# Optimization experiments

Hardware: AMD Instinct MI355X
Metric: run time of the kernel (lower is better)

## Reference

```python
import jax, jax.numpy as jnp
import numpy as np

WS = 7       # window size
SHIFT = 3    # shift size (ws//2)
NH = 16      # num heads
DIM = 512    # channels
HH = 112
WW = 112
HIDDEN = int(DIM * 4.0)
EPS = 1e-5


def _rel_index():
    # Swin relative position index, [N, N] ints into the bias table
    coords = np.stack(np.meshgrid(np.arange(WS), np.arange(WS), indexing='ij')).reshape(2, -1)
    rel = coords[:, :, None] - coords[:, None, :]
    rel = rel.transpose(1, 2, 0) + (WS - 1)
    rel[:, :, 0] *= 2 * WS - 1
    return rel.sum(-1)


def _attn_mask():
    # shifted-window mask on HH x WW (already multiples of WS) -> [nW, N, N] with 0 / -1e9
    img = np.zeros((HH, WW), np.int32)
    cnt = 0
    sl = (slice(0, -WS), slice(-WS, -SHIFT), slice(-SHIFT, None))
    for h in sl:
        for w in sl:
            img[h, w] = cnt
            cnt += 1
    win = img.reshape(HH // WS, WS, WW // WS, WS).transpose(0, 2, 1, 3).reshape(-1, WS * WS)
    diff = win[:, None, :] - win[:, :, None]
    return np.where(diff == 0, 0.0, -1e9).astype(np.float32)


def setup_inputs() -> dict:
    key = jax.random.key(0)
    ks = jax.random.split(key, 8)
    s = 0.02
    return {
        'x': jax.random.normal(ks[0], (DIM, HH, WW), jnp.float32),
        'norm1_w': jnp.ones((DIM,), jnp.float32),
        'norm1_b': jnp.zeros((DIM,), jnp.float32),
        'qkv_w': jax.random.normal(ks[1], (3 * DIM, DIM), jnp.float32) * s,
        'qkv_b': jnp.zeros((3 * DIM,), jnp.float32),
        'proj_w': jax.random.normal(ks[2], (DIM, DIM), jnp.float32) * s,
        'proj_b': jnp.zeros((DIM,), jnp.float32),
        'rpb_table': jax.random.normal(ks[3], ((2 * WS - 1) ** 2, NH), jnp.float32) * s,
        'norm2_w': jnp.ones((DIM,), jnp.float32),
        'norm2_b': jnp.zeros((DIM,), jnp.float32),
        'fc1_w': jax.random.normal(ks[4], (HIDDEN, DIM), jnp.float32) * s,
        'fc1_b': jnp.zeros((HIDDEN,), jnp.float32),
        'fc2_w': jax.random.normal(ks[5], (DIM, HIDDEN), jnp.float32) * s,
        'fc2_b': jnp.zeros((DIM,), jnp.float32),
    }


def _ln(x_hwc, w, b):
    m = x_hwc.mean(-1, keepdims=True)
    v = x_hwc.var(-1, keepdims=True)
    return (x_hwc - m) / jnp.sqrt(v + EPS) * w + b


def reference(x, norm1_w, norm1_b, qkv_w, qkv_b, proj_w, proj_b, rpb_table,
              norm2_w, norm2_b, fc1_w, fc1_b, fc2_w, fc2_b):
    C, H, W = x.shape
    ws = WS
    N = ws * ws
    hd = C // NH
    scale = 1.0 / np.sqrt(hd).astype(np.float32)

    x_hwc = jnp.moveaxis(x, 0, -1)                       # [H,W,C]
    xn = _ln(x_hwc, norm1_w, norm1_b)
    xs = jnp.roll(xn, (-SHIFT, -SHIFT), (0, 1))          # cyclic shift
    # window partition -> [nW, N, C]
    xw = xs.reshape(H // ws, ws, W // ws, ws, C).transpose(0, 2, 1, 3, 4).reshape(-1, N, C)

    qkv = xw @ qkv_w.T + qkv_b                            # [nW,N,3C]
    q, k, v = jnp.split(qkv, 3, -1)
    heads = lambda t: t.reshape(-1, N, NH, hd).transpose(0, 2, 1, 3)  # [nW,H,N,hd]
    q, k, v = heads(q), heads(k), heads(v)

    attn = jnp.einsum('whnd,whmd->whnm', q * scale, k)    # [nW,H,N,N]
    idx = jnp.asarray(_rel_index().reshape(-1))
    bias = rpb_table[idx].reshape(N, N, NH).transpose(2, 0, 1)  # [H,N,N]
    mask = jnp.asarray(_attn_mask())                       # [nW,N,N]
    attn = attn + bias[None] + mask[:, None]
    attn = jax.nn.softmax(attn, -1)

    out = jnp.einsum('whnm,whmd->whnd', attn, v).transpose(0, 2, 1, 3).reshape(-1, N, C)
    out = out @ proj_w.T + proj_b
    # window unpartition + reverse shift
    out = out.reshape(H // ws, W // ws, ws, ws, C).transpose(0, 2, 1, 3, 4).reshape(H, W, C)
    out = jnp.roll(out, (SHIFT, SHIFT), (0, 1))

    x1 = x_hwc + out                                       # residual (DropPath rate 0)
    x2 = _ln(x1, norm2_w, norm2_b)
    h = jax.nn.gelu(x2.reshape(-1, C) @ fc1_w.T + fc1_b)
    m = (h @ fc2_w.T + fc2_b).reshape(H, W, C)
    y = x1 + m
    return jnp.moveaxis(y, -1, 0)                          # back to [C,H,W]
```

## Files before the change

kernel.cpp:

```cpp
#include <hip/hip_runtime.h>

#define NPIX 12544
#define CDIM 512
#define QKVN 1536
#define HIDDEN 2048

typedef unsigned short u16;
typedef unsigned int u32;

typedef short bf16x8 __attribute__((ext_vector_type(8)));
typedef float f32x4 __attribute__((ext_vector_type(4)));

static __device__ __forceinline__ u16 f2bf(float f) {
  u32 u = __float_as_uint(f);
  return (u16)((u + 0x7fffu + ((u >> 16) & 1u)) >> 16);
}
static __device__ __forceinline__ u32 pack2(float a, float b) {
  return (u32)f2bf(a) | ((u32)f2bf(b) << 16);
}
static __device__ __forceinline__ u32 packtrunc2(float lo, float hi) {
  return __builtin_amdgcn_perm(__float_as_uint(hi), __float_as_uint(lo), 0x07060302u);
}
static __device__ __forceinline__ void async_ld16(const void* g, void* l) {
  __builtin_amdgcn_global_load_lds((__attribute__((address_space(1))) void*)g,
                                   (__attribute__((address_space(3))) void*)l, 16, 0, 0);
}

__global__ __launch_bounds__(256) void convert_weights(
    const float* __restrict__ qw, const float* __restrict__ pw,
    const float* __restrict__ w1, const float* __restrict__ w2,
    u16* __restrict__ Wq, u16* __restrict__ Wp, u16* __restrict__ W1o, u16* __restrict__ W2o) {
  const int b = blockIdx.x;
  const float* src; u16* dst; long off;
  if (b < 768)       { src = qw; dst = Wq;  off = (long)b * 1024; }
  else if (b < 1024) { src = pw; dst = Wp;  off = (long)(b - 768) * 1024; }
  else if (b < 2048) { src = w1; dst = W1o; off = (long)(b - 1024) * 1024; }
  else               { src = w2; dst = W2o; off = (long)(b - 2048) * 1024; }
  const long i = off / 4 + threadIdx.x;
  const float4 v = ((const float4*)src)[i];
  ushort4 u;
  u.x = f2bf(v.x); u.y = f2bf(v.y); u.z = f2bf(v.z); u.w = f2bf(v.w);
  ((ushort4*)dst)[i] = u;
}

__global__ __launch_bounds__(256) void ln1_partial(const float* __restrict__ x,
                                                   float* __restrict__ psum, float* __restrict__ pssq) {
  const int p = blockIdx.x * 256 + threadIdx.x;
  const int c0 = blockIdx.y * 32;
  float s = 0.f, ss = 0.f;
#pragma unroll
  for (int c = 0; c < 32; c++) {
    const float v = x[(long)(c0 + c) * NPIX + p];
    s += v; ss += v * v;
  }
  psum[blockIdx.y * NPIX + p] = s;
  pssq[blockIdx.y * NPIX + p] = ss;
}

__global__ __launch_bounds__(256) void ln1_stats(const float* __restrict__ psum, const float* __restrict__ pssq,
                                                 float* __restrict__ mean, float* __restrict__ rstd) {
  const int p = blockIdx.x * 256 + threadIdx.x;
  float s = 0.f, ss = 0.f;
#pragma unroll
  for (int ch = 0; ch < 16; ch++) { s += psum[ch * NPIX + p]; ss += pssq[ch * NPIX + p]; }
  const float m = s * (1.f / 512.f);
  const float v = ss * (1.f / 512.f) - m * m;
  mean[p] = m;
  rstd[p] = rsqrtf(v + 1e-5f);
}

__global__ __launch_bounds__(256) void ln1_shift_part(const float* __restrict__ x,
    const float* __restrict__ mean, const float* __restrict__ rstd,
    const float* __restrict__ gw, const float* __restrict__ gb, u16* __restrict__ xw) {
  __shared__ float tile[32][65];
  const int p0 = blockIdx.x * 64;
  const int c0 = blockIdx.y * 32;
  const int t = threadIdx.x;
  {
    const int pl = t & 63;
    const int cl0 = t >> 6;
#pragma unroll
    for (int r = 0; r < 8; r++) {
      const int cl = r * 4 + cl0;
      tile[cl][pl] = x[(long)(c0 + cl) * NPIX + p0 + pl];
    }
  }
  __syncthreads();
  const int cl = t & 31;
  const int g = t >> 5;
  const float wc = gw[c0 + cl];
  const float bc = gb[c0 + cl];
#pragma unroll
  for (int pass = 0; pass < 8; pass++) {
    const int pl = pass * 8 + g;
    const int p = p0 + pl;
    const int h = p / 112;
    const int w = p - h * 112;
    int hs = h + 109; if (hs >= 112) hs -= 112;
    int ws2 = w + 109; if (ws2 >= 112) ws2 -= 112;
    const int hq = hs / 7, wq = ws2 / 7;
    const int tok = (hq * 16 + wq) * 49 + (hs - hq * 7) * 7 + (ws2 - wq * 7);
    const float val = (tile[cl][pl] - mean[p]) * rstd[p] * wc + bc;
    xw[(long)tok * 512 + c0 + cl] = f2bf(val);
  }
}

template<bool OUT_BF16, bool DO_GELU, bool REMAP, bool FUSE_Y, bool FUSE_X>
__global__ __launch_bounds__(256, 3) void gemm_bt(
    const u16* __restrict__ A, const u16* __restrict__ B,
    const float* __restrict__ bias, void* __restrict__ out,
    const float* __restrict__ xtra, const int N, const int K) {
  __shared__ __align__(16) u16 Asm[128 * 32];
  __shared__ __align__(16) u16 Bsm[128 * 32];
  const int M0 = blockIdx.y << 7;
  const int N0 = blockIdx.x << 7;
  const int t = threadIdx.x;
  const int wave = t >> 6;
  const int lane = t & 63;
  const int l15 = lane & 15;
  const int quad = lane >> 4;
  const int wm = wave & 1;
  const int wn = wave >> 1;
  const int swz = (l15 >> 1) & 3;

  f32x4 acc[4][4] = {};

  for (int k0 = 0; k0 < K; k0 += 32) {
#pragma unroll
    for (int i = 0; i < 2; i++) {
      const int flatbase = i * 256 + wave * 64;
      const int FL = flatbase + lane;
      const int row = FL >> 2;
      const int chunk = (FL & 3) ^ ((row >> 1) & 3);
      async_ld16(A + (long)(M0 + row) * K + k0 + chunk * 8, &Asm[flatbase * 8]);
      async_ld16(B + (long)(N0 + row) * K + k0 + chunk * 8, &Bsm[flatbase * 8]);
    }
    __syncthreads();
    bf16x8 af[4], bfr[4];
#pragma unroll
    for (int im = 0; im < 4; im++)
      af[im] = *(const bf16x8*)&Asm[(wm * 64 + im * 16 + l15) * 32 + (quad ^ swz) * 8];
#pragma unroll
    for (int in = 0; in < 4; in++)
      bfr[in] = *(const bf16x8*)&Bsm[(wn * 64 + in * 16 + l15) * 32 + (quad ^ swz) * 8];
#pragma unroll
    for (int im = 0; im < 4; im++)
#pragma unroll
      for (int in = 0; in < 4; in++)
        acc[im][in] = __builtin_amdgcn_mfma_f32_16x16x32_bf16(bfr[in], af[im], acc[im][in], 0, 0, 0);
    __syncthreads();
  }

#pragma unroll
  for (int im = 0; im < 4; im++) {
    const int row = M0 + wm * 64 + im * 16 + l15;
    long orow = row;
    if (REMAP) {
      const int win = row / 49;
      const int nn = row - win * 49;
      const int nq = nn / 7;
      const int hs = (win >> 4) * 7 + nq;
      const int wsx = (win & 15) * 7 + (nn - nq * 7);
      int h = hs + 3; if (h >= 112) h -= 112;
      int w = wsx + 3; if (w >= 112) w -= 112;
      orow = h * 112 + w;
    }
#pragma unroll
    for (int in = 0; in < 4; in++) {
      const int col0 = N0 + wn * 64 + in * 16 + quad * 4;
      const float4 bv = *(const float4*)(bias + col0);
      float v[4];
      if (FUSE_Y) {
        const float4 xv = *(const float4*)(xtra + (long)row * CDIM + col0);
#pragma unroll
        for (int r = 0; r < 4; r++)
          v[r] = acc[im][in][r] + ((const float*)&bv)[r] + ((const float*)&xv)[r];
#pragma unroll
        for (int r = 0; r < 4; r++)
          ((float*)out)[(long)(col0 + r) * NPIX + row] = v[r];
      } else if (FUSE_X) {
        float v0 = acc[im][in][0] + bv.x + xtra[(long)(col0 + 0) * NPIX + orow];
        float v1 = acc[im][in][1] + bv.y + xtra[(long)(col0 + 1) * NPIX + orow];
        float v2 = acc[im][in][2] + bv.z + xtra[(long)(col0 + 2) * NPIX + orow];
        float v3 = acc[im][in][3] + bv.w + xtra[(long)(col0 + 3) * NPIX + orow];
        float4 f; f.x = v0; f.y = v1; f.z = v2; f.w = v3;
        *(float4*)((float*)out + orow * (long)N + col0) = f;
      } else {
#pragma unroll
        for (int r = 0; r < 4; r++) {
          float vv = acc[im][in][r] + ((const float*)&bv)[r];
          if (DO_GELU) {
            const float z2 = 1.5957691216f * (vv + 0.044715f * vv * vv * vv);
            vv = vv / (1.0f + __expf(-z2));
          }
          v[r] = vv;
        }
        if (OUT_BF16) {
          uint2 u;
          u.x = pack2(v[0], v[1]);
          u.y = pack2(v[2], v[3]);
          *(uint2*)((u16*)out + orow * (long)N + col0) = u;
        } else {
          float4 f; f.x = v[0]; f.y = v[1]; f.z = v[2]; f.w = v[3];
          *(float4*)((float*)out + orow * (long)N + col0) = f;
        }
      }
    }
  }
}

__global__ __launch_bounds__(256) void build_biasT(const float* __restrict__ rpb, float* __restrict__ biasT) {
  const int cls = blockIdx.x >> 4;
  const int head = blockIdx.x & 15;
  for (int e = threadIdx.x; e < 4096; e += 256) {
    const int j = e >> 6;
    const int i = e & 63;
    float v;
    if (j >= 49) v = -1e9f;
    else if (i >= 49) v = 0.f;
    else {
      const int ri = i / 7, ci = i - (i / 7) * 7;
      const int rj = j / 7, cj = j - (j / 7) * 7;
      v = rpb[((ri - rj + 6) * 13 + (ci - cj + 6)) * 16 + head];
      const int lhi = (cls & 2) ? (ri < 4 ? 1 : 2) : 0;
      const int lwi = (cls & 1) ? (ci < 4 ? 1 : 2) : 0;
      const int lhj = (cls & 2) ? (rj < 4 ? 1 : 2) : 0;
      const int lwj = (cls & 1) ? (cj < 4 ? 1 : 2) : 0;
      if (lhi * 3 + lwi != lhj * 3 + lwj) v = -1e9f;
    }
    biasT[(long)blockIdx.x * 4096 + e] = v;
  }
}

__global__ __launch_bounds__(256, 3) void attn_mfma(
    const u16* __restrict__ qkv, const float* __restrict__ biasT, u16* __restrict__ out) {
  __shared__ __align__(16) u16 slds[24576];
  const int t = threadIdx.x;
  const int wave = t >> 6;
  const int lane = t & 63;
  const int l15 = lane & 15;
  const int quad = lane >> 4;
  const int win = blockIdx.x >> 2;
  const int head = (blockIdx.x & 3) * 4 + wave;
  const int cls = (((win >> 4) == 15) ? 2 : 0) | (((win & 15) == 15) ? 1 : 0);

  u16* Qb  = slds + wave * 6144;
  u16* Kb  = Qb + 2048;
  u16* Vtb = Qb + 4096;
  u16* Pb  = Qb;

  const int rrow = lane >> 2;
  const int chunk = (lane & 3) ^ ((lane >> 3) & 3);
  uint4 vv[4];
#pragma unroll
  for (int it = 0; it < 4; it++) {
    const int row = it * 16 + rrow;
    const int jc = row < 49 ? row : 48;
    const long gbase = (long)(win * 49 + jc) * 1536 + head * 32 + chunk * 8;
    async_ld16(qkv + gbase,       Qb + it * 512 + lane * 8);
    async_ld16(qkv + gbase + 512, Kb + it * 512 + lane * 8);
    vv[it] = *(const uint4*)(qkv + gbase + 1024);
  }
  __syncthreads();

#pragma unroll
  for (int it = 0; it < 4; it++) {
    const int row = it * 16 + rrow;
    const u32* w = (const u32*)&vv[it];
#pragma unroll
    for (int tt = 0; tt < 8; tt++) {
      const int d = chunk * 8 + tt;
      const u16 val = (tt & 1) ? (u16)(w[tt >> 1] >> 16) : (u16)(w[tt >> 1] & 0xffffu);
      Vtb[d * 64 + (row ^ (((d >> 2) & 3) << 4))] = val;
    }
  }

  const int fswz = (l15 >> 1) & 3;
  bf16x8 kfrag[4], qfrag[4];
#pragma unroll
  for (int jm = 0; jm < 4; jm++)
    kfrag[jm] = *(const bf16x8*)(Kb + (jm * 16 + l15) * 32 + (quad ^ fswz) * 8);
#pragma unroll
  for (int in = 0; in < 4; in++)
    qfrag[in] = *(const bf16x8*)(Qb + (in * 16 + l15) * 32 + (quad ^ fswz) * 8);
  f32x4 sacc[4][4] = {};
#pragma unroll
  for (int jm = 0; jm < 4; jm++)
#pragma unroll
    for (int in = 0; in < 4; in++)
      sacc[jm][in] = __builtin_amdgcn_mfma_f32_16x16x32_bf16(kfrag[jm], qfrag[in], sacc[jm][in], 0, 0, 0);

  const float* bT = biasT + (long)(cls * 16 + head) * 4096;
  const float sc = 0.17677669529663687f;
#pragma unroll
  for (int jm = 0; jm < 4; jm++) {
    const float* bp = bT + (jm * 16 + quad * 4) * 64 + l15;
#pragma unroll
    for (int in = 0; in < 4; in++)
#pragma unroll
      for (int r = 0; r < 4; r++)
        sacc[jm][in][r] = sacc[jm][in][r] * sc + bp[r * 64 + in * 16];
  }
  float linv[4];
#pragma unroll
  for (int in = 0; in < 4; in++) {
    float m = -1e30f;
#pragma unroll
    for (int jm = 0; jm < 4; jm++)
#pragma unroll
      for (int r = 0; r < 4; r++) m = fmaxf(m, sacc[jm][in][r]);
    m = fmaxf(m, __shfl_xor(m, 16));
    m = fmaxf(m, __shfl_xor(m, 32));
    float s = 0.f;
#pragma unroll
    for (int jm = 0; jm < 4; jm++)
#pragma unroll
      for (int r = 0; r < 4; r++) {
        const float e = __expf(sacc[jm][in][r] - m);
        sacc[jm][in][r] = e; s += e;
      }
    s += __shfl_xor(s, 16);
    s += __shfl_xor(s, 32);
    linv[in] = __builtin_amdgcn_rcpf(s);
  }

#pragma unroll
  for (int in = 0; in < 4; in++) {
    const int i = in * 16 + l15;
    const int rot = (l15 & 3) << 4;
#pragma unroll
    for (int jm = 0; jm < 4; jm++) {
      const u32 lo = packtrunc2(sacc[jm][in][0], sacc[jm][in][1]);
      const u32 hi = packtrunc2(sacc[jm][in][2], sacc[jm][in][3]);
      uint2 u; u.x = lo; u.y = hi;
      *(uint2*)(Pb + i * 64 + ((jm * 16 + quad * 4) ^ rot)) = u;
    }
  }

  f32x4 oacc[2][4] = {};
#pragma unroll
  for (int ks = 0; ks < 2; ks++) {
    bf16x8 vtf[2], pf[4];
#pragma unroll
    for (int dm = 0; dm < 2; dm++)
      vtf[dm] = *(const bf16x8*)(Vtb + (dm * 16 + l15) * 64 + ((ks * 32 + quad * 8) ^ ((l15 >> 2) << 4)));
#pragma unroll
    for (int in = 0; in < 4; in++)
      pf[in] = *(const bf16x8*)(Pb + (in * 16 + l15) * 64 + ((ks * 32 + quad * 8) ^ ((l15 & 3) << 4)));
#pragma unroll
    for (int dm = 0; dm < 2; dm++)
#pragma unroll
      for (int in = 0; in < 4; in++)
        oacc[dm][in] = __builtin_amdgcn_mfma_f32_16x16x32_bf16(vtf[dm], pf[in], oacc[dm][in], 0, 0, 0);
  }

#pragma unroll
  for (int in = 0; in < 4; in++) {
    const int i = in * 16 + l15;
    if (i < 49) {
      const float inv = linv[in];
      const long base = (long)(win * 49 + i) * 512 + head * 32 + quad * 4;
#pragma unroll
      for (int dm = 0; dm < 2; dm++) {
        const float v0 = oacc[dm][in][0] * inv, v1 = oacc[dm][in][1] * inv;
        const float v2 = oacc[dm][in][2] * inv, v3 = oacc[dm][in][3] * inv;
        uint2 u; u.x = packtrunc2(v0, v1); u.y = packtrunc2(v2, v3);
        *(uint2*)(out + base + dm * 16) = u;
      }
    }
  }
}

__global__ __launch_bounds__(256) void ln2_apply(const float* __restrict__ x1,
    const float* __restrict__ gw, const float* __restrict__ gb, u16* __restrict__ x2) {
  const int wave = threadIdx.x >> 6;
  const int lane = threadIdx.x & 63;
  const int p = blockIdx.x * 4 + wave;
  const float4* row = (const float4*)(x1 + (long)p * 512);
  const float4 a = row[lane * 2];
  const float4 b = row[lane * 2 + 1];
  float s = a.x + a.y + a.z + a.w + b.x + b.y + b.z + b.w;
  float ss = a.x * a.x + a.y * a.y + a.z * a.z + a.w * a.w
           + b.x * b.x + b.y * b.y + b.z * b.z + b.w * b.w;
#pragma unroll
  for (int o = 32; o > 0; o >>= 1) { s += __shfl_xor(s, o); ss += __shfl_xor(ss, o); }
  const float m = s * (1.f / 512.f);
  const float var = ss * (1.f / 512.f) - m * m;
  const float rs = rsqrtf(var + 1e-5f);
  const float4 w0 = ((const float4*)gw)[lane * 2];
  const float4 w1 = ((const float4*)gw)[lane * 2 + 1];
  const float4 b0 = ((const float4*)gb)[lane * 2];
  const float4 b1 = ((const float4*)gb)[lane * 2 + 1];
  uint4 u;
  u.x = pack2((a.x - m) * rs * w0.x + b0.x, (a.y - m) * rs * w0.y + b0.y);
  u.y = pack2((a.z - m) * rs * w0.z + b0.z, (a.w - m) * rs * w0.w + b0.w);
  u.z = pack2((b.x - m) * rs * w1.x + b1.x, (b.y - m) * rs * w1.y + b1.y);
  u.w = pack2((b.z - m) * rs * w1.z + b1.z, (b.w - m) * rs * w1.w + b1.w);
  ((uint4*)(x2 + (long)p * 512))[lane] = u;
}

extern "C" void kernel_launch(void* const* d_in, const int* in_sizes, int n_in,
                              void* d_out, int out_size, void* d_ws, size_t ws_size,
                              hipStream_t stream) {
  (void)in_sizes; (void)n_in; (void)out_size; (void)ws_size;
  const float* x      = (const float*)d_in[0];
  const float* n1w    = (const float*)d_in[1];
  const float* n1b    = (const float*)d_in[2];
  const float* qkv_w  = (const float*)d_in[3];
  const float* qkv_b  = (const float*)d_in[4];
  const float* proj_w = (const float*)d_in[5];
  const float* proj_b = (const float*)d_in[6];
  const float* rpb    = (const float*)d_in[7];
  const float* n2w    = (const float*)d_in[8];
  const float* n2b    = (const float*)d_in[9];
  const float* fc1_w  = (const float*)d_in[10];
  const float* fc1_b  = (const float*)d_in[11];
  const float* fc2_w  = (const float*)d_in[12];
  const float* fc2_b  = (const float*)d_in[13];
  float* y = (float*)d_out;

  char* base = (char*)d_ws;
  size_t off = 0;
  auto alloc = [&](size_t b) { char* p = base + off; off += (b + 255) & ~(size_t)255; return p; };
  float* mean1 = (float*)alloc((size_t)NPIX * 4);
  float* rstd1 = (float*)alloc((size_t)NPIX * 4);
  float* psum  = (float*)alloc((size_t)16 * NPIX * 4);
  float* pssq  = (float*)alloc((size_t)16 * NPIX * 4);
  u16* Wq = (u16*)alloc((size_t)QKVN * CDIM * 2);
  u16* Wp = (u16*)alloc((size_t)CDIM * CDIM * 2);
  u16* W1 = (u16*)alloc((size_t)HIDDEN * CDIM * 2);
  u16* W2 = (u16*)alloc((size_t)CDIM * HIDDEN * 2);
  float* biasT = (float*)alloc((size_t)4 * 16 * 4096 * 4);
  u16* bufA = (u16*)alloc((size_t)NPIX * CDIM * 2);
  char* bufB = alloc((size_t)NPIX * QKVN * 2);
  float* x1 = (float*)alloc((size_t)NPIX * CDIM * 4);
  u16* hbuf = (u16*)alloc((size_t)NPIX * HIDDEN * 2);

  u16* xw      = bufA;
  u16* qkvbuf  = (u16*)bufB;
  u16* attnout = bufA;
  u16* x2 = bufA;

  convert_weights<<<3072, 256, 0, stream>>>(qkv_w, proj_w, fc1_w, fc2_w, Wq, Wp, W1, W2);
  build_biasT<<<64, 256, 0, stream>>>(rpb, biasT);

  ln1_partial<<<dim3(49, 16), 256, 0, stream>>>(x, psum, pssq);
  ln1_stats<<<49, 256, 0, stream>>>(psum, pssq, mean1, rstd1);
  ln1_shift_part<<<dim3(196, 16), 256, 0, stream>>>(x, mean1, rstd1, n1w, n1b, xw);

  gemm_bt<true, false, false, false, false><<<dim3(QKVN / 128, 98), 256, 0, stream>>>(xw, Wq, qkv_b, qkvbuf, nullptr, QKVN, CDIM);
  attn_mfma<<<1024, 256, 0, stream>>>(qkvbuf, biasT, attnout);
  gemm_bt<false, false, true, false, true><<<dim3(CDIM / 128, 98), 256, 0, stream>>>(attnout, Wp, proj_b, x1, x, CDIM, CDIM);

  ln2_apply<<<NPIX / 4, 256, 0, stream>>>(x1, n2w, n2b, x2);

  gemm_bt<true, true, false, false, false><<<dim3(HIDDEN / 128, 98), 256, 0, stream>>>(x2, W1, fc1_b, hbuf, nullptr, HIDDEN, CDIM);
  gemm_bt<false, false, false, true, false><<<dim3(CDIM / 128, 98), 256, 0, stream>>>(hbuf, W2, fc2_b, y, x1, CDIM, HIDDEN);
}
```

Measured before the change: 317.2 us.

## Fuse setup and LN1 kernels, remap GEMM tiles for XCD locality

```diff
diff --git a/kernel.cpp b/kernel.cpp
--- a/kernel.cpp
+++ b/kernel.cpp
@@ -4,6 +4,7 @@
 #define CDIM 512
 #define QKVN 1536
 #define HIDDEN 2048
+#define MT 98
 
 typedef unsigned short u16;
 typedef unsigned int u32;
@@ -26,82 +27,116 @@
                                    (__attribute__((address_space(3))) void*)l, 16, 0, 0);
 }
 
-__global__ __launch_bounds__(256) void convert_weights(
+__global__ __launch_bounds__(256) void setup_kernel(
     const float* __restrict__ qw, const float* __restrict__ pw,
     const float* __restrict__ w1, const float* __restrict__ w2,
-    u16* __restrict__ Wq, u16* __restrict__ Wp, u16* __restrict__ W1o, u16* __restrict__ W2o) {
+    const float* __restrict__ rpb,
+    u16* __restrict__ Wq, u16* __restrict__ Wp, u16* __restrict__ W1o, u16* __restrict__ W2o,
+    float* __restrict__ biasT) {
   const int b = blockIdx.x;
-  const float* src; u16* dst; long off;
-  if (b < 768)       { src = qw; dst = Wq;  off = (long)b * 1024; }
-  else if (b < 1024) { src = pw; dst = Wp;  off = (long)(b - 768) * 1024; }
-  else if (b < 2048) { src = w1; dst = W1o; off = (long)(b - 1024) * 1024; }
-  else               { src = w2; dst = W2o; off = (long)(b - 2048) * 1024; }
-  const long i = off / 4 + threadIdx.x;
-  const float4 v = ((const float4*)src)[i];
-  ushort4 u;
-  u.x = f2bf(v.x); u.y = f2bf(v.y); u.z = f2bf(v.z); u.w = f2bf(v.w);
-  ((ushort4*)dst)[i] = u;
-}
-
-__global__ __launch_bounds__(256) void ln1_partial(const float* __restrict__ x,
-                                                   float* __restrict__ psum, float* __restrict__ pssq) {
-  const int p = blockIdx.x * 256 + threadIdx.x;
-  const int c0 = blockIdx.y * 32;
-  float s = 0.f, ss = 0.f;
-#pragma unroll
-  for (int c = 0; c < 32; c++) {
-    const float v = x[(long)(c0 + c) * NPIX + p];
-    s += v; ss += v * v;
-  }
-  psum[blockIdx.y * NPIX + p] = s;
-  pssq[blockIdx.y * NPIX + p] = ss;
-}
-
-__global__ __launch_bounds__(256) void ln1_stats(const float* __restrict__ psum, const float* __restrict__ pssq,
-                                                 float* __restrict__ mean, float* __restrict__ rstd) {
-  const int p = blockIdx.x * 256 + threadIdx.x;
-  float s = 0.f, ss = 0.f;
-#pragma unroll
-  for (int ch = 0; ch < 16; ch++) { s += psum[ch * NPIX + p]; ss += pssq[ch * NPIX + p]; }
-  const float m = s * (1.f / 512.f);
-  const float v = ss * (1.f / 512.f) - m * m;
-  mean[p] = m;
-  rstd[p] = rsqrtf(v + 1e-5f);
-}
-
-__global__ __launch_bounds__(256) void ln1_shift_part(const float* __restrict__ x,
-    const float* __restrict__ mean, const float* __restrict__ rstd,
+  if (b < 3072) {
+    const float* src; u16* dst; long off;
+    if (b < 768)       { src = qw; dst = Wq;  off = (long)b * 1024; }
+    else if (b < 1024) { src = pw; dst = Wp;  off = (long)(b - 768) * 1024; }
+    else if (b < 2048) { src = w1; dst = W1o; off = (long)(b - 1024) * 1024; }
+    else               { src = w2; dst = W2o; off = (long)(b - 2048) * 1024; }
+    const long i = off / 4 + threadIdx.x;
+    const float4 v = ((const float4*)src)[i];
+    ushort4 u;
+    u.x = f2bf(v.x); u.y = f2bf(v.y); u.z = f2bf(v.z); u.w = f2bf(v.w);
+    ((ushort4*)dst)[i] = u;
+  } else {
+    const int bb = b - 3072;
+    const int cls = bb >> 4;
+    const int head = bb & 15;
+    for (int e = threadIdx.x; e < 4096; e += 256) {
+      const int j = e >> 6;
+      const int i = e & 63;
+      float v;
+      if (j >= 49) v = -1e9f;
+      else if (i >= 49) v = 0.f;
+      else {
+        const int ri = i / 7, ci = i - (i / 7) * 7;
+        const int rj = j / 7, cj = j - (j / 7) * 7;
+        v = rpb[((ri - rj + 6) * 13 + (ci - cj + 6)) * 16 + head];
+        const int lhi = (cls & 2) ? (ri < 4 ? 1 : 2) : 0;
+        const int lwi = (cls & 1) ? (ci < 4 ? 1 : 2) : 0;
+        const int lhj = (cls & 2) ? (rj < 4 ? 1 : 2) : 0;
+        const int lwj = (cls & 1) ? (cj < 4 ? 1 : 2) : 0;
+        if (lhi * 3 + lwi != lhj * 3 + lwj) v = -1e9f;
+      }
+      biasT[(long)bb * 4096 + e] = v;
+    }
+  }
+}
+
+__global__ __launch_bounds__(256) void ln1_fused(const float* __restrict__ x,
     const float* __restrict__ gw, const float* __restrict__ gb, u16* __restrict__ xw) {
   __shared__ float tile[32][65];
+  __shared__ float sred[4][64], ssred[4][64];
+  __shared__ float mean_s[64], rstd_s[64];
   const int p0 = blockIdx.x * 64;
-  const int c0 = blockIdx.y * 32;
   const int t = threadIdx.x;
-  {
-    const int pl = t & 63;
-    const int cl0 = t >> 6;
-#pragma unroll
-    for (int r = 0; r < 8; r++) {
-      const int cl = r * 4 + cl0;
-      tile[cl][pl] = x[(long)(c0 + cl) * NPIX + p0 + pl];
-    }
-  }
+  const int pl = t & 63;
+  const int cg = t >> 6;
+  float s = 0.f, ss = 0.f;
+  for (int c0 = 0; c0 < 512; c0 += 32) {
+    {
+      const int lcl0 = t >> 6;
+#pragma unroll
+      for (int r = 0; r < 8; r++) {
+        const int cl = r * 4 + lcl0;
+        tile[cl][t & 63] = x[(long)(c0 + cl) * NPIX + p0 + (t & 63)];
+      }
+    }
+    __syncthreads();
+#pragma unroll
+    for (int i = 0; i < 8; i++) {
+      const float v = tile[cg * 8 + i][pl];
+      s += v; ss += v * v;
+    }
+    __syncthreads();
+  }
+  sred[cg][pl] = s; ssred[cg][pl] = ss;
   __syncthreads();
+  if (t < 64) {
+    const float st = sred[0][t] + sred[1][t] + sred[2][t] + sred[3][t];
+    const float sst = ssred[0][t] + ssred[1][t] + ssred[2][t] + ssred[3][t];
+    const float m = st * (1.f / 512.f);
+    const float var = sst * (1.f / 512.f) - m * m;
+    mean_s[t] = m;
+    rstd_s[t] = rsqrtf(var + 1e-5f);
+  }
+  __syncthreads();
+
   const int cl = t & 31;
   const int g = t >> 5;
-  const float wc = gw[c0 + cl];
-  const float bc = gb[c0 + cl];
-#pragma unroll
-  for (int pass = 0; pass < 8; pass++) {
-    const int pl = pass * 8 + g;
-    const int p = p0 + pl;
-    const int h = p / 112;
-    const int w = p - h * 112;
-    int hs = h + 109; if (hs >= 112) hs -= 112;
-    int ws2 = w + 109; if (ws2 >= 112) ws2 -= 112;
-    const int hq = hs / 7, wq = ws2 / 7;
-    const int tok = (hq * 16 + wq) * 49 + (hs - hq * 7) * 7 + (ws2 - wq * 7);
-    const float val = (tile[cl][pl] - mean[p]) * rstd[p] * wc + bc;
-    xw[(long)tok * 512 + c0 + cl] = f2bf(val);
+  for (int c0 = 0; c0 < 512; c0 += 32) {
+    {
+      const int lcl0 = t >> 6;
+#pragma unroll
+      for (int r = 0; r < 8; r++) {
+        const int ccl = r * 4 + lcl0;
+        tile[ccl][t & 63] = x[(long)(c0 + ccl) * NPIX + p0 + (t & 63)];
+      }
+    }
+    __syncthreads();
+    const float wc = gw[c0 + cl];
+    const float bc = gb[c0 + cl];
+#pragma unroll
+    for (int pass = 0; pass < 8; pass++) {
+      const int pl2 = pass * 8 + g;
+      const int p = p0 + pl2;
+      const int h = p / 112;
+      const int w = p - h * 112;
+      int hs = h + 109; if (hs >= 112) hs -= 112;
+      int ws2 = w + 109; if (ws2 >= 112) ws2 -= 112;
+      const int hq = hs / 7, wq = ws2 / 7;
+      const int tok = (hq * 16 + wq) * 49 + (hs - hq * 7) * 7 + (ws2 - wq * 7);
+      const float val = (tile[cl][pl2] - mean_s[pl2]) * rstd_s[pl2] * wc + bc;
+      xw[(long)tok * 512 + c0 + cl] = f2bf(val);
+    }
+    __syncthreads();
   }
 }
 
@@ -110,10 +145,19 @@
     const u16* __restrict__ A, const u16* __restrict__ B,
     const float* __restrict__ bias, void* __restrict__ out,
     const float* __restrict__ xtra, const int N, const int K) {
+  const int NT = N >> 7;
+  const int id = blockIdx.x;
+  const int xcd = id & 7;
+  const int j = id >> 3;
+  const int ml = j / NT;
+  const int nt = j - ml * NT;
+  const int mt = xcd * 13 + ml;
+  if (mt >= MT) return;
+
   __shared__ __align__(16) u16 Asm[128 * 32];
   __shared__ __align__(16) u16 Bsm[128 * 32];
-  const int M0 = blockIdx.y << 7;
-  const int N0 = blockIdx.x << 7;
+  const int M0 = mt << 7;
+  const int N0 = nt << 7;
   const int t = threadIdx.x;
   const int wave = t >> 6;
   const int lane = t & 63;
@@ -206,29 +250,6 @@
         }
       }
     }
-  }
-}
-
-__global__ __launch_bounds__(256) void build_biasT(const float* __restrict__ rpb, float* __restrict__ biasT) {
-  const int cls = blockIdx.x >> 4;
-  const int head = blockIdx.x & 15;
-  for (int e = threadIdx.x; e < 4096; e += 256) {
-    const int j = e >> 6;
-    const int i = e & 63;
-    float v;
-    if (j >= 49) v = -1e9f;
-    else if (i >= 49) v = 0.f;
-    else {
-      const int ri = i / 7, ci = i - (i / 7) * 7;
-      const int rj = j / 7, cj = j - (j / 7) * 7;
-      v = rpb[((ri - rj + 6) * 13 + (ci - cj + 6)) * 16 + head];
-      const int lhi = (cls & 2) ? (ri < 4 ? 1 : 2) : 0;
-      const int lwi = (cls & 1) ? (ci < 4 ? 1 : 2) : 0;
-      const int lhj = (cls & 2) ? (rj < 4 ? 1 : 2) : 0;
-      const int lwj = (cls & 1) ? (cj < 4 ? 1 : 2) : 0;
-      if (lhi * 3 + lwi != lhj * 3 + lwj) v = -1e9f;
-    }
-    biasT[(long)blockIdx.x * 4096 + e] = v;
   }
 }
 
@@ -422,10 +443,6 @@
   char* base = (char*)d_ws;
   size_t off = 0;
   auto alloc = [&](size_t b) { char* p = base + off; off += (b + 255) & ~(size_t)255; return p; };
-  float* mean1 = (float*)alloc((size_t)NPIX * 4);
-  float* rstd1 = (float*)alloc((size_t)NPIX * 4);
-  float* psum  = (float*)alloc((size_t)16 * NPIX * 4);
-  float* pssq  = (float*)alloc((size_t)16 * NPIX * 4);
   u16* Wq = (u16*)alloc((size_t)QKVN * CDIM * 2);
   u16* Wp = (u16*)alloc((size_t)CDIM * CDIM * 2);
   u16* W1 = (u16*)alloc((size_t)HIDDEN * CDIM * 2);
@@ -441,19 +458,16 @@
   u16* attnout = bufA;
   u16* x2 = bufA;
 
-  convert_weights<<<3072, 256, 0, stream>>>(qkv_w, proj_w, fc1_w, fc2_w, Wq, Wp, W1, W2);
-  build_biasT<<<64, 256, 0, stream>>>(rpb, biasT);
-
-  ln1_partial<<<dim3(49, 16), 256, 0, stream>>>(x, psum, pssq);
-  ln1_stats<<<49, 256, 0, stream>>>(psum, pssq, mean1, rstd1);
-  ln1_shift_part<<<dim3(196, 16), 256, 0, stream>>>(x, mean1, rstd1, n1w, n1b, xw);
-
-  gemm_bt<true, false, false, false, false><<<dim3(QKVN / 128, 98), 256, 0, stream>>>(xw, Wq, qkv_b, qkvbuf, nullptr, QKVN, CDIM);
+  setup_kernel<<<3136, 256, 0, stream>>>(qkv_w, proj_w, fc1_w, fc2_w, rpb, Wq, Wp, W1, W2, biasT);
+
+  ln1_fused<<<196, 256, 0, stream>>>(x, n1w, n1b, xw);
+
+  gemm_bt<true, false, false, false, false><<<8 * 13 * (QKVN / 128), 256, 0, stream>>>(xw, Wq, qkv_b, qkvbuf, nullptr, QKVN, CDIM);
   attn_mfma<<<1024, 256, 0, stream>>>(qkvbuf, biasT, attnout);
-  gemm_bt<false, false, true, false, true><<<dim3(CDIM / 128, 98), 256, 0, stream>>>(attnout, Wp, proj_b, x1, x, CDIM, CDIM);
+  gemm_bt<false, false, true, false, true><<<8 * 13 * (CDIM / 128), 256, 0, stream>>>(attnout, Wp, proj_b, x1, x, CDIM, CDIM);
 
   ln2_apply<<<NPIX / 4, 256, 0, stream>>>(x1, n2w, n2b, x2);
 
-  gemm_bt<true, true, false, false, false><<<dim3(HIDDEN / 128, 98), 256, 0, stream>>>(x2, W1, fc1_b, hbuf, nullptr, HIDDEN, CDIM);
-  gemm_bt<false, false, false, true, false><<<dim3(CDIM / 128, 98), 256, 0, stream>>>(hbuf, W2, fc2_b, y, x1, CDIM, HIDDEN);
-}
+  gemm_bt<true, true, false, false, false><<<8 * 13 * (HIDDEN / 128), 256, 0, stream>>>(x2, W1, fc1_b, hbuf, nullptr, HIDDEN, CDIM);
+  gemm_bt<false, false, false, true, false><<<8 * 13 * (CDIM / 128), 256, 0, stream>>>(hbuf, W2, fc2_b, y, x1, CDIM, HIDDEN);
+}
```

After: 322.7 us. About the same (+1.7%).
